# Optimization experiments

Measured on AMD Instinct MI355X. Metric: run time of the kernel, lower is better.

The kernel has to match this reference:

```python
import jax, jax.numpy as jnp
import numpy as np

B, T, R, D = 8, 32, 512, 256

def quat_conjugate(q):
    return q * jnp.array([1.0, -1.0, -1.0, -1.0], dtype=q.dtype)

def quat_multiply(q1, q2):
    w1, x1, y1, z1 = q1[..., 0], q1[..., 1], q1[..., 2], q1[..., 3]
    w2, x2, y2, z2 = q2[..., 0], q2[..., 1], q2[..., 2], q2[..., 3]
    return jnp.stack([
        w1 * w2 - x1 * x2 - y1 * y2 - z1 * z2,
        w1 * x2 + x1 * w2 + y1 * z2 - z1 * y2,
        w1 * y2 - x1 * z2 + y1 * w2 + z1 * x2,
        w1 * z2 + x1 * y2 - y1 * x2 + z1 * w2], axis=-1)

def quat_to_matrix(q):
    q = q / (jnp.linalg.norm(q, axis=-1, keepdims=True) + 1e-8)
    w, x, y, z = q[..., 0], q[..., 1], q[..., 2], q[..., 3]
    return jnp.stack([
        jnp.stack([1 - 2 * (y * y + z * z), 2 * (x * y - w * z), 2 * (x * z + w * y)], -1),
        jnp.stack([2 * (x * y + w * z), 1 - 2 * (x * x + z * z), 2 * (y * z - w * x)], -1),
        jnp.stack([2 * (x * z - w * y), 2 * (y * z + w * x), 1 - 2 * (x * x + y * y)], -1)], axis=-2)

def rotate_vector(q, v):
    return jnp.einsum('...ij,...j->...i', quat_to_matrix(q), v)

def setup_inputs() -> dict:
    key = jax.random.key(0)
    ks = jax.random.split(key, 8)
    s = lambda fan_in: 1.0 / np.sqrt(fan_in)
    return {
        'scalar_features': jax.random.normal(ks[0], (B, T, D), jnp.float32),
        'quat': jax.random.normal(ks[1], (B, T, R, 4), jnp.float32),
        'trans': jax.random.normal(ks[2], (B, T, R, 3), jnp.float32),
        'W1': jax.random.normal(ks[3], (D + 3, D), jnp.float32) * s(D + 3),
        'b1': jnp.zeros((D,), jnp.float32),
        'W2': jax.random.normal(ks[4], (D, D // 2), jnp.float32) * s(D),
        'b2': jnp.zeros((D // 2,), jnp.float32),
        'Wt': jax.random.normal(ks[5], (D // 2, 3), jnp.float32) * s(D // 2),
        'bt': jnp.zeros((3,), jnp.float32),
        'Wr': jax.random.normal(ks[6], (D // 2, 3), jnp.float32) * s(D // 2),
        'br': jnp.zeros((3,), jnp.float32),
    }

def reference(scalar_features, quat, trans, W1, b1, W2, b2, Wt, bt, Wr, br):
    b, t, r, _ = trans.shape
    d = scalar_features.shape[-1]
    x = jnp.broadcast_to(scalar_features[:, :, None, :], (b, t, r, d))
    centroid = jnp.mean(trans, axis=2, keepdims=True)
    rel_pos = trans - centroid
    local_rel_pos = rotate_vector(quat_conjugate(quat), rel_pos)
    x = jnp.concatenate([x, local_rel_pos], axis=-1)          # (B,T,R,d+3)
    x = jax.nn.gelu(x @ W1 + b1)                               # (B,T,R,d)
    x = jax.nn.gelu(x @ W2 + b2)                               # (B,T,R,d//2)
    trans_vel = rotate_vector(quat, x @ Wt + bt)               # (B,T,R,3)
    rot_vel_local = (x @ Wr + br) * 0.1
    omega_quat = jnp.concatenate([jnp.zeros((b, t, r, 1), x.dtype), rot_vel_local], axis=-1)
    quat_vel = 0.5 * quat_multiply(quat, omega_quat)
    return jnp.concatenate([quat_vel, trans_vel], axis=-1)    # (B,T,R,7)
```

## Files before the change

### kernel.cpp

```cpp
#include <hip/hip_runtime.h>
#include <math.h>

#define GB 256
#define RR 512
#define DD 256
#define DH 128
#define NTHREADS 512

typedef __bf16 bf16x8 __attribute__((ext_vector_type(8)));
typedef unsigned short u16x8 __attribute__((ext_vector_type(8)));
typedef float f32x4 __attribute__((ext_vector_type(4)));

#define OFF_LRP  0u
#define OFF_BASE 2097152u
#define OFF_W2F  2359296u
#define OFF_WB   2424832u
#define WS_NEED  2428928u

__device__ __forceinline__ float fast_gelu(float x) {
    float t = x * x;
    float m = x * fmaf(t, -0.10294325f, -2.30220820f);
    float e = __builtin_amdgcn_exp2f(m);
    return x * __builtin_amdgcn_rcpf(1.0f + e);
}

__device__ __forceinline__ unsigned short bf_bits(float x) {
    union { float f; unsigned u; } c; c.f = x;
    unsigned r = c.u + 0x7FFFu + ((c.u >> 16) & 1u);
    return (unsigned short)(r >> 16);
}

__global__ __launch_bounds__(NTHREADS, 2)
void prep_kernel(const float* __restrict__ SF, const float* __restrict__ Q,
                 const float* __restrict__ TR, const float* __restrict__ W1,
                 const float* __restrict__ b1, const float* __restrict__ W2,
                 const float* __restrict__ Wt, const float* __restrict__ Wr,
                 float* __restrict__ wsLrp, float* __restrict__ wsBase,
                 unsigned short* __restrict__ wsW2f, unsigned short* __restrict__ wsWB)
{
    const int bx = blockIdx.x;
    const int t = threadIdx.x;

    if (bx == GB) {
        #pragma unroll 2
        for (int idx = t; idx < 4096; idx += NTHREADS) {
            int pair = idx >> 6, lane = idx & 63;
            int wv2 = pair >> 3, ks = pair & 7;
            int ln = lane & 15, lq = lane >> 4;
            int col = (wv2 << 4) | ln;
            u16x8 tmp;
            #pragma unroll
            for (int i = 0; i < 8; ++i)
                tmp[i] = bf_bits(W2[(ks * 32 + lq * 8 + i) * DH + col]);
            *(u16x8*)&wsW2f[idx * 8] = tmp;
        }
        for (int idx = t; idx < 2048; idx += NTHREADS) {
            int ks = idx >> 9, rem = idx & 511;
            int lane = rem >> 3, i = rem & 7;
            int bq = (lane >> 4) & 3, bn = lane & 15;
            int k = ks * 32 + bq * 8 + i;
            float v = (bn < 3) ? Wt[k * 3 + bn] : (bn < 6 ? Wr[k * 3 + bn - 3] : 0.0f);
            wsWB[idx] = bf_bits(v);
        }
        return;
    }

    const int g = bx;
    __shared__ float sRed[8][4];
    __shared__ float sCent[3];
    __shared__ float sS[DD];
    __shared__ float sPart[8 * DD];

    const float* trp = TR + ((size_t)g * RR + t) * 3;
    float rx = trp[0], ry = trp[1], rz = trp[2];
    const float4 q = ((const float4*)Q)[(size_t)g * RR + t];
    if (t < 64) ((float4*)sS)[t] = ((const float4*)(SF + (size_t)g * DD))[t];

    float sx = rx, sy = ry, sz = rz;
    #pragma unroll
    for (int d = 1; d < 64; d <<= 1) {
        sx += __shfl_xor(sx, d); sy += __shfl_xor(sy, d); sz += __shfl_xor(sz, d);
    }
    const int wv = t >> 6, wl = t & 63;
    if (wl == 0) { sRed[wv][0] = sx; sRed[wv][1] = sy; sRed[wv][2] = sz; }
    __syncthreads();
    if (t == 0) {
        float cx = 0, cy = 0, cz = 0;
        #pragma unroll
        for (int i = 0; i < 8; ++i) { cx += sRed[i][0]; cy += sRed[i][1]; cz += sRed[i][2]; }
        sCent[0] = cx * (1.0f / RR); sCent[1] = cy * (1.0f / RR); sCent[2] = cz * (1.0f / RR);
    }

    {
        const int jg = t & 63, ks = t >> 6;
        const int j4 = jg * 4, k0 = ks * 32;
        float4 acc = {0.f, 0.f, 0.f, 0.f};
        #pragma unroll 8
        for (int kk = 0; kk < 32; ++kk) {
            float s = sS[k0 + kk];
            float4 w = *(const float4*)&W1[(size_t)(k0 + kk) * DD + j4];
            acc.x = fmaf(s, w.x, acc.x);
            acc.y = fmaf(s, w.y, acc.y);
            acc.z = fmaf(s, w.z, acc.z);
            acc.w = fmaf(s, w.w, acc.w);
        }
        *(float4*)&sPart[ks * DD + j4] = acc;
    }
    __syncthreads();

    if (t < DD) {
        float a = b1[t];
        #pragma unroll
        for (int i = 0; i < 8; ++i) a += sPart[i * DD + t];
        wsBase[(size_t)g * DD + t] = a;
    }

    {
        float ax = rx - sCent[0], ay = ry - sCent[1], az = rz - sCent[2];
        float qw = q.x, qx = q.y, qy = q.z, qz = q.w;
        float n = sqrtf(qw * qw + qx * qx + qy * qy + qz * qz) + 1e-8f;
        float inv = 1.0f / n;
        float nw = qw * inv, nx = qx * inv, ny = qy * inv, nz = qz * inv;
        float xx = nx * nx, yy = ny * ny, zz = nz * nz;
        float xy = nx * ny, xz = nx * nz, yz = ny * nz;
        float wx = nw * nx, wy = nw * ny, wz = nw * nz;
        float m00 = 1.f - 2.f * (yy + zz), m01 = 2.f * (xy - wz), m02 = 2.f * (xz + wy);
        float m10 = 2.f * (xy + wz), m11 = 1.f - 2.f * (xx + zz), m12 = 2.f * (yz - wx);
        float m20 = 2.f * (xz - wy), m21 = 2.f * (yz + wx), m22 = 1.f - 2.f * (xx + yy);
        float4 o;
        o.x = m00 * ax + m10 * ay + m20 * az;
        o.y = m01 * ax + m11 * ay + m21 * az;
        o.z = m02 * ax + m12 * ay + m22 * az;
        o.w = 0.0f;
        ((float4*)wsLrp)[(size_t)g * RR + t] = o;
    }
}

__global__ __launch_bounds__(NTHREADS, 6)
void main_kernel(const float* __restrict__ Q, const float* __restrict__ W1,
                 const float* __restrict__ b2, const float* __restrict__ bt,
                 const float* __restrict__ br,
                 const float* __restrict__ wsLrp, const float* __restrict__ wsBase,
                 const unsigned short* __restrict__ wsW2f,
                 const unsigned short* __restrict__ wsWB,
                 float* __restrict__ out)
{
    __shared__ unsigned short sH1u[64 * 264];
    __shared__ float sDot[64][6];

    const int bx = blockIdx.x;
    const int g = bx >> 3;
    const int r0 = (bx & 7) << 6;
    const int t = threadIdx.x;
    const int wv = t >> 6, wl = t & 63, ln = t & 15, lq = (t >> 4) & 3;
    const int colN = (wv << 4) | ln;
    unsigned short* sH2b = sH1u;

    bf16x8 Breg[8];
    #pragma unroll
    for (int ks = 0; ks < 8; ++ks)
        Breg[ks] = *(const bf16x8*)&wsW2f[((wv * 8 + ks) * 64 + wl) * 8];

    const int l4 = wl * 4;
    const float4 base4 = *(const float4*)&wsBase[g * DD + l4];
    const float4 w1ta = *(const float4*)&W1[256 * DD + l4];
    const float4 w1tb = *(const float4*)&W1[257 * DD + l4];
    const float4 w1tc = *(const float4*)&W1[258 * DD + l4];
    const float bb = b2[colN];

    #pragma unroll
    for (int it = 0; it < 8; ++it) {
        int row = wv * 8 + it;
        float4 l = ((const float4*)wsLrp)[(size_t)g * RR + r0 + row];
        float v0 = base4.x + l.x * w1ta.x + l.y * w1tb.x + l.z * w1tc.x;
        float v1 = base4.y + l.x * w1ta.y + l.y * w1tb.y + l.z * w1tc.y;
        float v2 = base4.z + l.x * w1ta.z + l.y * w1tb.z + l.z * w1tc.z;
        float v3 = base4.w + l.x * w1ta.w + l.y * w1tb.w + l.z * w1tc.w;
        unsigned p0 = (unsigned)bf_bits(fast_gelu(v0)) | ((unsigned)bf_bits(fast_gelu(v1)) << 16);
        unsigned p1 = (unsigned)bf_bits(fast_gelu(v2)) | ((unsigned)bf_bits(fast_gelu(v3)) << 16);
        uint2 pk; pk.x = p0; pk.y = p1;
        *(uint2*)&sH1u[row * 264 + l4] = pk;
    }
    __syncthreads();

    f32x4 acc0 = {0.f, 0.f, 0.f, 0.f};
    f32x4 acc1 = {0.f, 0.f, 0.f, 0.f};
    f32x4 acc2 = {0.f, 0.f, 0.f, 0.f};
    f32x4 acc3 = {0.f, 0.f, 0.f, 0.f};
    {
        const unsigned short* aBase = sH1u + ln * 264 + lq * 8;
        #pragma unroll
        for (int ks = 0; ks < 8; ++ks) {
            bf16x8 b = Breg[ks];
            bf16x8 a0 = *(const bf16x8*)(aBase + ks * 32);
            bf16x8 a1 = *(const bf16x8*)(aBase + 16 * 264 + ks * 32);
            bf16x8 a2 = *(const bf16x8*)(aBase + 32 * 264 + ks * 32);
            bf16x8 a3 = *(const bf16x8*)(aBase + 48 * 264 + ks * 32);
            acc0 = __builtin_amdgcn_mfma_f32_16x16x32_bf16(a0, b, acc0, 0, 0, 0);
            acc1 = __builtin_amdgcn_mfma_f32_16x16x32_bf16(a1, b, acc1, 0, 0, 0);
            acc2 = __builtin_amdgcn_mfma_f32_16x16x32_bf16(a2, b, acc2, 0, 0, 0);
            acc3 = __builtin_amdgcn_mfma_f32_16x16x32_bf16(a3, b, acc3, 0, 0, 0);
        }
    }
    __syncthreads();

    #pragma unroll
    for (int r = 0; r < 4; ++r) {
        int rq = lq * 4 + r;
        sH2b[(rq)      * 136 + colN] = bf_bits(fast_gelu(acc0[r] + bb));
        sH2b[(rq + 16) * 136 + colN] = bf_bits(fast_gelu(acc1[r] + bb));
        sH2b[(rq + 32) * 136 + colN] = bf_bits(fast_gelu(acc2[r] + bb));
        sH2b[(rq + 48) * 136 + colN] = bf_bits(fast_gelu(acc3[r] + bb));
    }
    __syncthreads();

    if (wv < 4) {
        f32x4 dacc = {0.f, 0.f, 0.f, 0.f};
        const unsigned short* aB = sH2b + (wv * 16 + ln) * 136 + lq * 8;
        #pragma unroll
        for (int ks = 0; ks < 4; ++ks) {
            bf16x8 a = *(const bf16x8*)(aB + ks * 32);
            bf16x8 b = *(const bf16x8*)(&wsWB[ks * 512 + wl * 8]);
            dacc = __builtin_amdgcn_mfma_f32_16x16x32_bf16(a, b, dacc, 0, 0, 0);
        }
        if (ln < 6) {
            #pragma unroll
            for (int r = 0; r < 4; ++r)
                sDot[wv * 16 + lq * 4 + r][ln] = dacc[r];
        }
        if (wl < 16) {
            int row = wv * 16 + wl;
            float4 q = ((const float4*)Q)[(size_t)g * RR + r0 + row];
            float qw = q.x, qx = q.y, qy = q.z, qz = q.w;
            float n = sqrtf(qw * qw + qx * qx + qy * qy + qz * qz) + 1e-8f;
            float inv = 1.0f / n;
            float nw = qw * inv, nx = qx * inv, ny = qy * inv, nz = qz * inv;
            float tvp0 = sDot[row][0] + bt[0];
            float tvp1 = sDot[row][1] + bt[1];
            float tvp2 = sDot[row][2] + bt[2];
            float rv0 = (sDot[row][3] + br[0]) * 0.1f;
            float rv1 = (sDot[row][4] + br[1]) * 0.1f;
            float rv2 = (sDot[row][5] + br[2]) * 0.1f;
            float xx = nx * nx, yy = ny * ny, zz = nz * nz;
            float xy = nx * ny, xz = nx * nz, yz = ny * nz;
            float wx = nw * nx, wy = nw * ny, wz = nw * nz;
            float m00 = 1.f - 2.f * (yy + zz), m01 = 2.f * (xy - wz), m02 = 2.f * (xz + wy);
            float m10 = 2.f * (xy + wz), m11 = 1.f - 2.f * (xx + zz), m12 = 2.f * (yz - wx);
            float m20 = 2.f * (xz - wy), m21 = 2.f * (yz + wx), m22 = 1.f - 2.f * (xx + yy);
            float tv0 = m00 * tvp0 + m01 * tvp1 + m02 * tvp2;
            float tv1 = m10 * tvp0 + m11 * tvp1 + m12 * tvp2;
            float tv2 = m20 * tvp0 + m21 * tvp1 + m22 * tvp2;
            float* op = out + ((size_t)g * RR + r0 + row) * 7;
            op[0] = -0.5f * (qx * rv0 + qy * rv1 + qz * rv2);
            op[1] =  0.5f * (qw * rv0 + qy * rv2 - qz * rv1);
            op[2] =  0.5f * (qw * rv1 - qx * rv2 + qz * rv0);
            op[3] =  0.5f * (qw * rv2 + qx * rv1 - qy * rv0);
            op[4] = tv0; op[5] = tv1; op[6] = tv2;
        }
    }
}

__global__ __launch_bounds__(NTHREADS, 4)
void eq_head_fallback(const float* __restrict__ SF, const float* __restrict__ Q,
                      const float* __restrict__ TR, const float* __restrict__ W1,
                      const float* __restrict__ b1, const float* __restrict__ W2,
                      const float* __restrict__ b2, const float* __restrict__ Wt,
                      const float* __restrict__ bt, const float* __restrict__ Wr,
                      const float* __restrict__ br, float* __restrict__ out)
{
    __shared__ char sBuf[64 * 264 * 2];
    __shared__ float sLrp[RR][3];
    __shared__ float sS[DD];
    __shared__ float sW1t[3][DD];
    __shared__ float sBase[DD];
    __shared__ float sB2[DH];
    __shared__ unsigned short sWB[4 * 512];
    __shared__ float sDot[64][6];
    __shared__ float sCent[3];
    __shared__ float sBt[3];
    __shared__ float sBr[3];

    unsigned short* sH1u = (unsigned short*)sBuf;
    unsigned short* sH2b = (unsigned short*)sBuf;
    float* scratch = (float*)sBuf;

    const int g = blockIdx.x;
    const int t = threadIdx.x;
    const int wv = t >> 6, wl = t & 63, ln = t & 15, lq = (t >> 4) & 3;
    const int colN = (wv << 4) + ln;

    if (t < DD) sS[t] = SF[g * DD + t];
    for (int idx = t; idx < 3 * DD; idx += NTHREADS)
        ((float*)sW1t)[idx] = W1[DD * DD + idx];
    if (t < DH) sB2[t] = b2[t];
    if (t < 3) { sBt[t] = bt[t]; sBr[t] = br[t]; }
    for (int idx = t; idx < 2048; idx += NTHREADS) {
        int ks = idx >> 9, rem = idx & 511;
        int lane = rem >> 3, i = rem & 7;
        int bq = (lane >> 4) & 3, bn = lane & 15;
        int k = ks * 32 + bq * 8 + i;
        float v = (bn < 3) ? Wt[k * 3 + bn] : (bn < 6 ? Wr[k * 3 + bn - 3] : 0.0f);
        sWB[idx] = bf_bits(v);
    }
    {
        const float* trp = TR + ((size_t)g * RR + t) * 3;
        scratch[t] = trp[0]; scratch[512 + t] = trp[1]; scratch[1024 + t] = trp[2];
    }
    __syncthreads();
    for (int s = 256; s > 0; s >>= 1) {
        if (t < s) {
            scratch[t] += scratch[t + s];
            scratch[512 + t] += scratch[512 + t + s];
            scratch[1024 + t] += scratch[1024 + t + s];
        }
        __syncthreads();
    }
    if (t < 3) sCent[t] = scratch[t * 512] * (1.0f / RR);
    __syncthreads();
    {
        const float4 q = ((const float4*)Q)[(size_t)g * RR + t];
        const float* trp = TR + ((size_t)g * RR + t) * 3;
        float rx = trp[0] - sCent[0], ry = trp[1] - sCent[1], rz = trp[2] - sCent[2];
        float qw = q.x, qx = q.y, qy = q.z, qz = q.w;
        float n = sqrtf(qw * qw + qx * qx + qy * qy + qz * qz) + 1e-8f;
        float inv = 1.0f / n;
        float nw = qw * inv, nx = qx * inv, ny = qy * inv, nz = qz * inv;
        float xx = nx * nx, yy = ny * ny, zz = nz * nz;
        float xy = nx * ny, xz = nx * nz, yz = ny * nz;
        float wx = nw * nx, wy = nw * ny, wz = nw * nz;
        float m00 = 1.f - 2.f * (yy + zz), m01 = 2.f * (xy - wz), m02 = 2.f * (xz + wy);
        float m10 = 2.f * (xy + wz), m11 = 1.f - 2.f * (xx + zz), m12 = 2.f * (yz - wx);
        float m20 = 2.f * (xz - wy), m21 = 2.f * (yz + wx), m22 = 1.f - 2.f * (xx + yy);
        sLrp[t][0] = m00 * rx + m10 * ry + m20 * rz;
        sLrp[t][1] = m01 * rx + m11 * ry + m21 * rz;
        sLrp[t][2] = m02 * rx + m12 * ry + m22 * rz;
    }
    {
        const int j = t & 255, half = t >> 8;
        float acc0 = 0.0f;
        for (int k = half * 128; k < half * 128 + 128; ++k)
            acc0 += sS[k] * W1[k * DD + j];
        __syncthreads();
        scratch[t] = acc0;
        __syncthreads();
        if (t < DD) sBase[t] = scratch[t] + scratch[DD + t] + b1[t];
    }
    bf16x8 Breg[8];
    #pragma unroll
    for (int ks = 0; ks < 8; ++ks) {
        u16x8 tmp;
        #pragma unroll
        for (int i = 0; i < 8; ++i)
            tmp[i] = bf_bits(W2[(ks * 32 + lq * 8 + i) * DH + colN]);
        Breg[ks] = __builtin_bit_cast(bf16x8, tmp);
    }
    __syncthreads();
    const int l4 = wl * 4;
    float4 base4 = *(const float4*)&sBase[l4];
    float4 w1ta = *(const float4*)&sW1t[0][l4];
    float4 w1tb = *(const float4*)&sW1t[1][l4];
    float4 w1tc = *(const float4*)&sW1t[2][l4];
    const float4* Qv = (const float4*)Q + (size_t)g * RR;
    const int cfirst = blockIdx.y * 4;
    for (int cc = 0; cc < 4; ++cc) {
        const int r0 = (cfirst + cc) * 64;
        #pragma unroll
        for (int it = 0; it < 8; ++it) {
            int row = wv * 8 + it;
            float l0 = sLrp[r0 + row][0], l1 = sLrp[r0 + row][1], l2 = sLrp[r0 + row][2];
            float v0 = base4.x + l0 * w1ta.x + l1 * w1tb.x + l2 * w1tc.x;
            float v1 = base4.y + l0 * w1ta.y + l1 * w1tb.y + l2 * w1tc.y;
            float v2 = base4.z + l0 * w1ta.z + l1 * w1tb.z + l2 * w1tc.z;
            float v3 = base4.w + l0 * w1ta.w + l1 * w1tb.w + l2 * w1tc.w;
            unsigned p0 = (unsigned)bf_bits(fast_gelu(v0)) | ((unsigned)bf_bits(fast_gelu(v1)) << 16);
            unsigned p1 = (unsigned)bf_bits(fast_gelu(v2)) | ((unsigned)bf_bits(fast_gelu(v3)) << 16);
            uint2 pk; pk.x = p0; pk.y = p1;
            *(uint2*)&sH1u[row * 264 + l4] = pk;
        }
        __syncthreads();
        f32x4 acc0 = {0,0,0,0}, acc1 = {0,0,0,0}, acc2 = {0,0,0,0}, acc3 = {0,0,0,0};
        {
            const unsigned short* aBase = sH1u + ln * 264 + lq * 8;
            #pragma unroll
            for (int ks = 0; ks < 8; ++ks) {
                bf16x8 b = Breg[ks];
                bf16x8 a0 = *(const bf16x8*)(aBase + ks * 32);
                bf16x8 a1 = *(const bf16x8*)(aBase + 16 * 264 + ks * 32);
                bf16x8 a2 = *(const bf16x8*)(aBase + 32 * 264 + ks * 32);
                bf16x8 a3 = *(const bf16x8*)(aBase + 48 * 264 + ks * 32);
                acc0 = __builtin_amdgcn_mfma_f32_16x16x32_bf16(a0, b, acc0, 0, 0, 0);
                acc1 = __builtin_amdgcn_mfma_f32_16x16x32_bf16(a1, b, acc1, 0, 0, 0);
                acc2 = __builtin_amdgcn_mfma_f32_16x16x32_bf16(a2, b, acc2, 0, 0, 0);
                acc3 = __builtin_amdgcn_mfma_f32_16x16x32_bf16(a3, b, acc3, 0, 0, 0);
            }
        }
        __syncthreads();
        {
            float bb = sB2[colN];
            #pragma unroll
            for (int r = 0; r < 4; ++r) {
                int rq = lq * 4 + r;
                sH2b[(rq) * 136 + colN] = bf_bits(fast_gelu(acc0[r] + bb));
                sH2b[(rq + 16) * 136 + colN] = bf_bits(fast_gelu(acc1[r] + bb));
                sH2b[(rq + 32) * 136 + colN] = bf_bits(fast_gelu(acc2[r] + bb));
                sH2b[(rq + 48) * 136 + colN] = bf_bits(fast_gelu(acc3[r] + bb));
            }
        }
        __syncthreads();
        if (wv < 4) {
            f32x4 dacc = {0,0,0,0};
            const unsigned short* aB = sH2b + (wv * 16 + ln) * 136 + lq * 8;
            #pragma unroll
            for (int ks = 0; ks < 4; ++ks) {
                bf16x8 a = *(const bf16x8*)(aB + ks * 32);
                bf16x8 b = *(const bf16x8*)(&sWB[ks * 512 + wl * 8]);
                dacc = __builtin_amdgcn_mfma_f32_16x16x32_bf16(a, b, dacc, 0, 0, 0);
            }
            if (ln < 6) {
                #pragma unroll
                for (int r = 0; r < 4; ++r)
                    sDot[wv * 16 + lq * 4 + r][ln] = dacc[r];
            }
        }
        __syncthreads();
        if (t < 64) {
            float4 q = Qv[r0 + t];
            float qw = q.x, qx = q.y, qy = q.z, qz = q.w;
            float n = sqrtf(qw * qw + qx * qx + qy * qy + qz * qz) + 1e-8f;
            float inv = 1.0f / n;
            float nw = qw * inv, nx = qx * inv, ny = qy * inv, nz = qz * inv;
            float tvp0 = sDot[t][0] + sBt[0];
            float tvp1 = sDot[t][1] + sBt[1];
            float tvp2 = sDot[t][2] + sBt[2];
            float rv0 = (sDot[t][3] + sBr[0]) * 0.1f;
            float rv1 = (sDot[t][4] + sBr[1]) * 0.1f;
            float rv2 = (sDot[t][5] + sBr[2]) * 0.1f;
            float xx = nx * nx, yy = ny * ny, zz = nz * nz;
            float xy = nx * ny, xz = nx * nz, yz = ny * nz;
            float wx = nw * nx, wy = nw * ny, wz = nw * nz;
            float m00 = 1.f - 2.f * (yy + zz), m01 = 2.f * (xy - wz), m02 = 2.f * (xz + wy);
            float m10 = 2.f * (xy + wz), m11 = 1.f - 2.f * (xx + zz), m12 = 2.f * (yz - wx);
            float m20 = 2.f * (xz - wy), m21 = 2.f * (yz + wx), m22 = 1.f - 2.f * (xx + yy);
            float tv0 = m00 * tvp0 + m01 * tvp1 + m02 * tvp2;
            float tv1 = m10 * tvp0 + m11 * tvp1 + m12 * tvp2;
            float tv2 = m20 * tvp0 + m21 * tvp1 + m22 * tvp2;
            float* op = out + ((size_t)g * RR + r0 + t) * 7;
            op[0] = -0.5f * (qx * rv0 + qy * rv1 + qz * rv2);
            op[1] =  0.5f * (qw * rv0 + qy * rv2 - qz * rv1);
            op[2] =  0.5f * (qw * rv1 - qx * rv2 + qz * rv0);
            op[3] =  0.5f * (qw * rv2 + qx * rv1 - qy * rv0);
            op[4] = tv0; op[5] = tv1; op[6] = tv2;
        }
        __syncthreads();
    }
}

extern "C" void kernel_launch(void* const* d_in, const int* in_sizes, int n_in,
                              void* d_out, int out_size, void* d_ws, size_t ws_size,
                              hipStream_t stream) {
    const float* SF = (const float*)d_in[0];
    const float* Q  = (const float*)d_in[1];
    const float* TR = (const float*)d_in[2];
    const float* W1 = (const float*)d_in[3];
    const float* b1 = (const float*)d_in[4];
    const float* W2 = (const float*)d_in[5];
    const float* b2 = (const float*)d_in[6];
    const float* Wt = (const float*)d_in[7];
    const float* bt = (const float*)d_in[8];
    const float* Wr = (const float*)d_in[9];
    const float* br = (const float*)d_in[10];
    float* out = (float*)d_out;

    if (ws_size >= WS_NEED) {
        char* ws = (char*)d_ws;
        float* wsLrp = (float*)(ws + OFF_LRP);
        float* wsBase = (float*)(ws + OFF_BASE);
        unsigned short* wsW2f = (unsigned short*)(ws + OFF_W2F);
        unsigned short* wsWB = (unsigned short*)(ws + OFF_WB);
        prep_kernel<<<GB + 1, NTHREADS, 0, stream>>>(SF, Q, TR, W1, b1, W2, Wt, Wr,
                                                     wsLrp, wsBase, wsW2f, wsWB);
        main_kernel<<<GB * 8, NTHREADS, 0, stream>>>(Q, W1, b2, bt, br,
                                                     wsLrp, wsBase, wsW2f, wsWB, out);
    } else {
        dim3 grid(GB, 2);
        eq_head_fallback<<<grid, NTHREADS, 0, stream>>>(SF, Q, TR, W1, b1, W2, b2,
                                                        Wt, bt, Wr, br, out);
    }
}
```

Measured before the change: 107.6 us.

## Process two row chunks per block, stage WB in LDS, use packed bf16 convert

Each main_kernel block now loops over two 64-row chunks of the same group, so the grid is halved and the per-block setup (W2 fragment registers, base and W1 tail vectors, bias) is reused across both chunks. The small WB projection matrix is copied once into shared memory instead of being read from global memory per chunk. The bf16 packing of the first GELU output uses the hardware packed convert builtin when it is available. Fewer blocks mean less parallelism per CU and an extra barrier per chunk, and the hardware convert may round differently from the manual path.

```diff
diff --git a/kernel.cpp b/kernel.cpp
--- a/kernel.cpp
+++ b/kernel.cpp
@@ -28,6 +28,15 @@
     union { float f; unsigned u; } c; c.f = x;
     unsigned r = c.u + 0x7FFFu + ((c.u >> 16) & 1u);
     return (unsigned short)(r >> 16);
+}
+
+__device__ __forceinline__ unsigned pack_bf16(float a, float b) {
+#if __has_builtin(__builtin_amdgcn_cvt_pk_bf16_f32)
+    auto p = __builtin_amdgcn_cvt_pk_bf16_f32(a, b);
+    return __builtin_bit_cast(unsigned, p);
+#else
+    return (unsigned)bf_bits(a) | ((unsigned)bf_bits(b) << 16);
+#endif
 }
 
 __global__ __launch_bounds__(NTHREADS, 2)
@@ -146,15 +155,18 @@
                  float* __restrict__ out)
 {
     __shared__ unsigned short sH1u[64 * 264];
+    __shared__ unsigned short sWB[2048];
     __shared__ float sDot[64][6];
 
     const int bx = blockIdx.x;
-    const int g = bx >> 3;
-    const int r0 = (bx & 7) << 6;
+    const int g = bx >> 2;
+    const int ch0 = (bx & 3) << 1;
     const int t = threadIdx.x;
     const int wv = t >> 6, wl = t & 63, ln = t & 15, lq = (t >> 4) & 3;
     const int colN = (wv << 4) | ln;
     unsigned short* sH2b = sH1u;
+
+    if (t < 256) ((uint4*)sWB)[t] = ((const uint4*)wsWB)[t];
 
     bf16x8 Breg[8];
     #pragma unroll
@@ -168,95 +180,100 @@
     const float4 w1tc = *(const float4*)&W1[258 * DD + l4];
     const float bb = b2[colN];
 
-    #pragma unroll
-    for (int it = 0; it < 8; ++it) {
-        int row = wv * 8 + it;
-        float4 l = ((const float4*)wsLrp)[(size_t)g * RR + r0 + row];
-        float v0 = base4.x + l.x * w1ta.x + l.y * w1tb.x + l.z * w1tc.x;
-        float v1 = base4.y + l.x * w1ta.y + l.y * w1tb.y + l.z * w1tc.y;
-        float v2 = base4.z + l.x * w1ta.z + l.y * w1tb.z + l.z * w1tc.z;
-        float v3 = base4.w + l.x * w1ta.w + l.y * w1tb.w + l.z * w1tc.w;
-        unsigned p0 = (unsigned)bf_bits(fast_gelu(v0)) | ((unsigned)bf_bits(fast_gelu(v1)) << 16);
-        unsigned p1 = (unsigned)bf_bits(fast_gelu(v2)) | ((unsigned)bf_bits(fast_gelu(v3)) << 16);
-        uint2 pk; pk.x = p0; pk.y = p1;
-        *(uint2*)&sH1u[row * 264 + l4] = pk;
-    }
-    __syncthreads();
-
-    f32x4 acc0 = {0.f, 0.f, 0.f, 0.f};
-    f32x4 acc1 = {0.f, 0.f, 0.f, 0.f};
-    f32x4 acc2 = {0.f, 0.f, 0.f, 0.f};
-    f32x4 acc3 = {0.f, 0.f, 0.f, 0.f};
-    {
-        const unsigned short* aBase = sH1u + ln * 264 + lq * 8;
+    for (int cc = 0; cc < 2; ++cc) {
+        const int r0 = (ch0 + cc) << 6;
+
         #pragma unroll
-        for (int ks = 0; ks < 8; ++ks) {
-            bf16x8 b = Breg[ks];
-            bf16x8 a0 = *(const bf16x8*)(aBase + ks * 32);
-            bf16x8 a1 = *(const bf16x8*)(aBase + 16 * 264 + ks * 32);
-            bf16x8 a2 = *(const bf16x8*)(aBase + 32 * 264 + ks * 32);
-            bf16x8 a3 = *(const bf16x8*)(aBase + 48 * 264 + ks * 32);
-            acc0 = __builtin_amdgcn_mfma_f32_16x16x32_bf16(a0, b, acc0, 0, 0, 0);
-            acc1 = __builtin_amdgcn_mfma_f32_16x16x32_bf16(a1, b, acc1, 0, 0, 0);
-            acc2 = __builtin_amdgcn_mfma_f32_16x16x32_bf16(a2, b, acc2, 0, 0, 0);
-            acc3 = __builtin_amdgcn_mfma_f32_16x16x32_bf16(a3, b, acc3, 0, 0, 0);
-        }
-    }
-    __syncthreads();
-
-    #pragma unroll
-    for (int r = 0; r < 4; ++r) {
-        int rq = lq * 4 + r;
-        sH2b[(rq)      * 136 + colN] = bf_bits(fast_gelu(acc0[r] + bb));
-        sH2b[(rq + 16) * 136 + colN] = bf_bits(fast_gelu(acc1[r] + bb));
-        sH2b[(rq + 32) * 136 + colN] = bf_bits(fast_gelu(acc2[r] + bb));
-        sH2b[(rq + 48) * 136 + colN] = bf_bits(fast_gelu(acc3[r] + bb));
-    }
-    __syncthreads();
-
-    if (wv < 4) {
-        f32x4 dacc = {0.f, 0.f, 0.f, 0.f};
-        const unsigned short* aB = sH2b + (wv * 16 + ln) * 136 + lq * 8;
+        for (int it = 0; it < 8; ++it) {
+            int row = wv * 8 + it;
+            float4 l = ((const float4*)wsLrp)[(size_t)g * RR + r0 + row];
+            float v0 = base4.x + l.x * w1ta.x + l.y * w1tb.x + l.z * w1tc.x;
+            float v1 = base4.y + l.x * w1ta.y + l.y * w1tb.y + l.z * w1tc.y;
+            float v2 = base4.z + l.x * w1ta.z + l.y * w1tb.z + l.z * w1tc.z;
+            float v3 = base4.w + l.x * w1ta.w + l.y * w1tb.w + l.z * w1tc.w;
+            uint2 pk;
+            pk.x = pack_bf16(fast_gelu(v0), fast_gelu(v1));
+            pk.y = pack_bf16(fast_gelu(v2), fast_gelu(v3));
+            *(uint2*)&sH1u[row * 264 + l4] = pk;
+        }
+        __syncthreads();
+
+        f32x4 acc0 = {0.f, 0.f, 0.f, 0.f};
+        f32x4 acc1 = {0.f, 0.f, 0.f, 0.f};
+        f32x4 acc2 = {0.f, 0.f, 0.f, 0.f};
+        f32x4 acc3 = {0.f, 0.f, 0.f, 0.f};
+        {
+            const unsigned short* aBase = sH1u + ln * 264 + lq * 8;
+            #pragma unroll
+            for (int ks = 0; ks < 8; ++ks) {
+                bf16x8 b = Breg[ks];
+                bf16x8 a0 = *(const bf16x8*)(aBase + ks * 32);
+                bf16x8 a1 = *(const bf16x8*)(aBase + 16 * 264 + ks * 32);
+                bf16x8 a2 = *(const bf16x8*)(aBase + 32 * 264 + ks * 32);
+                bf16x8 a3 = *(const bf16x8*)(aBase + 48 * 264 + ks * 32);
+                acc0 = __builtin_amdgcn_mfma_f32_16x16x32_bf16(a0, b, acc0, 0, 0, 0);
+                acc1 = __builtin_amdgcn_mfma_f32_16x16x32_bf16(a1, b, acc1, 0, 0, 0);
+                acc2 = __builtin_amdgcn_mfma_f32_16x16x32_bf16(a2, b, acc2, 0, 0, 0);
+                acc3 = __builtin_amdgcn_mfma_f32_16x16x32_bf16(a3, b, acc3, 0, 0, 0);
+            }
+        }
+        __syncthreads();
+
         #pragma unroll
-        for (int ks = 0; ks < 4; ++ks) {
-            bf16x8 a = *(const bf16x8*)(aB + ks * 32);
-            bf16x8 b = *(const bf16x8*)(&wsWB[ks * 512 + wl * 8]);
-            dacc = __builtin_amdgcn_mfma_f32_16x16x32_bf16(a, b, dacc, 0, 0, 0);
-        }
-        if (ln < 6) {
+        for (int r = 0; r < 4; ++r) {
+            int rq = lq * 4 + r;
+            sH2b[(rq)      * 136 + colN] = bf_bits(fast_gelu(acc0[r] + bb));
+            sH2b[(rq + 16) * 136 + colN] = bf_bits(fast_gelu(acc1[r] + bb));
+            sH2b[(rq + 32) * 136 + colN] = bf_bits(fast_gelu(acc2[r] + bb));
+            sH2b[(rq + 48) * 136 + colN] = bf_bits(fast_gelu(acc3[r] + bb));
+        }
+        __syncthreads();
+
+        if (wv < 4) {
+            f32x4 dacc = {0.f, 0.f, 0.f, 0.f};
+            const unsigned short* aB = sH2b + (wv * 16 + ln) * 136 + lq * 8;
             #pragma unroll
-            for (int r = 0; r < 4; ++r)
-                sDot[wv * 16 + lq * 4 + r][ln] = dacc[r];
-        }
-        if (wl < 16) {
-            int row = wv * 16 + wl;
-            float4 q = ((const float4*)Q)[(size_t)g * RR + r0 + row];
-            float qw = q.x, qx = q.y, qy = q.z, qz = q.w;
-            float n = sqrtf(qw * qw + qx * qx + qy * qy + qz * qz) + 1e-8f;
-            float inv = 1.0f / n;
-            float nw = qw * inv, nx = qx * inv, ny = qy * inv, nz = qz * inv;
-            float tvp0 = sDot[row][0] + bt[0];
-            float tvp1 = sDot[row][1] + bt[1];
-            float tvp2 = sDot[row][2] + bt[2];
-            float rv0 = (sDot[row][3] + br[0]) * 0.1f;
-            float rv1 = (sDot[row][4] + br[1]) * 0.1f;
-            float rv2 = (sDot[row][5] + br[2]) * 0.1f;
-            float xx = nx * nx, yy = ny * ny, zz = nz * nz;
-            float xy = nx * ny, xz = nx * nz, yz = ny * nz;
-            float wx = nw * nx, wy = nw * ny, wz = nw * nz;
-            float m00 = 1.f - 2.f * (yy + zz), m01 = 2.f * (xy - wz), m02 = 2.f * (xz + wy);
-            float m10 = 2.f * (xy + wz), m11 = 1.f - 2.f * (xx + zz), m12 = 2.f * (yz - wx);
-            float m20 = 2.f * (xz - wy), m21 = 2.f * (yz + wx), m22 = 1.f - 2.f * (xx + yy);
-            float tv0 = m00 * tvp0 + m01 * tvp1 + m02 * tvp2;
-            float tv1 = m10 * tvp0 + m11 * tvp1 + m12 * tvp2;
-            float tv2 = m20 * tvp0 + m21 * tvp1 + m22 * tvp2;
-            float* op = out + ((size_t)g * RR + r0 + row) * 7;
-            op[0] = -0.5f * (qx * rv0 + qy * rv1 + qz * rv2);
-            op[1] =  0.5f * (qw * rv0 + qy * rv2 - qz * rv1);
-            op[2] =  0.5f * (qw * rv1 - qx * rv2 + qz * rv0);
-            op[3] =  0.5f * (qw * rv2 + qx * rv1 - qy * rv0);
-            op[4] = tv0; op[5] = tv1; op[6] = tv2;
-        }
+            for (int ks = 0; ks < 4; ++ks) {
+                bf16x8 a = *(const bf16x8*)(aB + ks * 32);
+                bf16x8 b = *(const bf16x8*)(&sWB[ks * 512 + wl * 8]);
+                dacc = __builtin_amdgcn_mfma_f32_16x16x32_bf16(a, b, dacc, 0, 0, 0);
+            }
+            if (ln < 6) {
+                #pragma unroll
+                for (int r = 0; r < 4; ++r)
+                    sDot[wv * 16 + lq * 4 + r][ln] = dacc[r];
+            }
+            if (wl < 16) {
+                int row = wv * 16 + wl;
+                float4 q = ((const float4*)Q)[(size_t)g * RR + r0 + row];
+                float qw = q.x, qx = q.y, qy = q.z, qz = q.w;
+                float n = sqrtf(qw * qw + qx * qx + qy * qy + qz * qz) + 1e-8f;
+                float inv = 1.0f / n;
+                float nw = qw * inv, nx = qx * inv, ny = qy * inv, nz = qz * inv;
+                float tvp0 = sDot[row][0] + bt[0];
+                float tvp1 = sDot[row][1] + bt[1];
+                float tvp2 = sDot[row][2] + bt[2];
+                float rv0 = (sDot[row][3] + br[0]) * 0.1f;
+                float rv1 = (sDot[row][4] + br[1]) * 0.1f;
+                float rv2 = (sDot[row][5] + br[2]) * 0.1f;
+                float xx = nx * nx, yy = ny * ny, zz = nz * nz;
+                float xy = nx * ny, xz = nx * nz, yz = ny * nz;
+                float wx = nw * nx, wy = nw * ny, wz = nw * nz;
+                float m00 = 1.f - 2.f * (yy + zz), m01 = 2.f * (xy - wz), m02 = 2.f * (xz + wy);
+                float m10 = 2.f * (xy + wz), m11 = 1.f - 2.f * (xx + zz), m12 = 2.f * (yz - wx);
+                float m20 = 2.f * (xz - wy), m21 = 2.f * (yz + wx), m22 = 1.f - 2.f * (xx + yy);
+                float tv0 = m00 * tvp0 + m01 * tvp1 + m02 * tvp2;
+                float tv1 = m10 * tvp0 + m11 * tvp1 + m12 * tvp2;
+                float tv2 = m20 * tvp0 + m21 * tvp1 + m22 * tvp2;
+                float* op = out + ((size_t)g * RR + r0 + row) * 7;
+                op[0] = -0.5f * (qx * rv0 + qy * rv1 + qz * rv2);
+                op[1] =  0.5f * (qw * rv0 + qy * rv2 - qz * rv1);
+                op[2] =  0.5f * (qw * rv1 - qx * rv2 + qz * rv0);
+                op[3] =  0.5f * (qw * rv2 + qx * rv1 - qy * rv0);
+                op[4] = tv0; op[5] = tv1; op[6] = tv2;
+            }
+        }
+        __syncthreads();
     }
 }
 
@@ -372,9 +389,9 @@
             float v1 = base4.y + l0 * w1ta.y + l1 * w1tb.y + l2 * w1tc.y;
             float v2 = base4.z + l0 * w1ta.z + l1 * w1tb.z + l2 * w1tc.z;
             float v3 = base4.w + l0 * w1ta.w + l1 * w1tb.w + l2 * w1tc.w;
-            unsigned p0 = (unsigned)bf_bits(fast_gelu(v0)) | ((unsigned)bf_bits(fast_gelu(v1)) << 16);
-            unsigned p1 = (unsigned)bf_bits(fast_gelu(v2)) | ((unsigned)bf_bits(fast_gelu(v3)) << 16);
-            uint2 pk; pk.x = p0; pk.y = p1;
+            uint2 pk;
+            pk.x = pack_bf16(fast_gelu(v0), fast_gelu(v1));
+            pk.y = pack_bf16(fast_gelu(v2), fast_gelu(v3));
             *(uint2*)&sH1u[row * 264 + l4] = pk;
         }
         __syncthreads();
@@ -479,7 +496,7 @@
         unsigned short* wsWB = (unsigned short*)(ws + OFF_WB);
         prep_kernel<<<GB + 1, NTHREADS, 0, stream>>>(SF, Q, TR, W1, b1, W2, Wt, Wr,
                                                      wsLrp, wsBase, wsW2f, wsWB);
-        main_kernel<<<GB * 8, NTHREADS, 0, stream>>>(Q, W1, b2, bt, br,
+        main_kernel<<<GB * 4, NTHREADS, 0, stream>>>(Q, W1, b2, bt, br,
                                                      wsLrp, wsBase, wsW2f, wsWB, out);
     } else {
         dim3 grid(GB, 2);
```

Measured after the change: 120.0 us. 1.12x slower.
